# Kernel optimization log

Measured on AMD Instinct MI355X. Metric: run time of the kernel, lower is better.

The kernel has to match this reference:

```python
import jax, jax.numpy as jnp
import numpy as np

NUM_HEADS = 16
HEAD_DIM = 64


def setup_inputs() -> dict:
    key = jax.random.key(0)
    k1, k2, k3 = jax.random.split(key, 3)
    B, N, D = 4, 2048, NUM_HEADS * HEAD_DIM
    q = jax.random.normal(k1, (B, N, D), dtype=jnp.float32)
    k = jax.random.normal(k2, (B, N, D), dtype=jnp.float32)
    v = jax.random.normal(k3, (B, N, D), dtype=jnp.float32)
    # causal mask: True where attention is allowed
    attn_mask = jnp.tril(jnp.ones((N, N), dtype=bool))
    return {"q": q, "k": k, "v": v, "attn_mask": attn_mask}


def reference(q, k, v, attn_mask):
    B, N, D = q.shape
    H, Hd = NUM_HEADS, HEAD_DIM
    # [B, N, H*Hd] -> [B, H, N, Hd]
    qh = q.reshape(B, N, H, Hd).transpose(0, 2, 1, 3)
    kh = k.reshape(B, N, H, Hd).transpose(0, 2, 1, 3)
    vh = v.reshape(B, N, H, Hd).transpose(0, 2, 1, 3)
    scale = 1.0 / jnp.sqrt(jnp.asarray(Hd, dtype=q.dtype))
    scores = jnp.einsum('bhqd,bhkd->bhqk', qh, kh) * scale  # [B,H,N,N]
    scores = jnp.where(attn_mask[None, None, :, :], scores, -jnp.inf)
    probs = jax.nn.softmax(scores, axis=-1)
    y = jnp.einsum('bhqk,bhkd->bhqd', probs, vh)  # [B,H,N,Hd]
    return y.transpose(0, 2, 1, 3).reshape(B, N, H * Hd)
```

## Files before the change

### kernel.cpp

```cpp
#include <hip/hip_runtime.h>

#define RS 1024
#define SEQLEN 2048

typedef __fp16 f16;
typedef __attribute__((ext_vector_type(2))) __fp16 half2v;
typedef __attribute__((ext_vector_type(4))) __fp16 half4v;
typedef __attribute__((ext_vector_type(8))) __fp16 half8v;
typedef __attribute__((ext_vector_type(4))) float float4v;

__device__ __forceinline__ half8v pack8h(float4v a, float4v b) {
  union { half8v v; half2v h[4]; } u;
  u.h[0] = __builtin_amdgcn_cvt_pkrtz(a[0], a[1]);
  u.h[1] = __builtin_amdgcn_cvt_pkrtz(a[2], a[3]);
  u.h[2] = __builtin_amdgcn_cvt_pkrtz(b[0], b[1]);
  u.h[3] = __builtin_amdgcn_cvt_pkrtz(b[2], b[3]);
  return u.v;
}

template<int NG, bool DOMASK>
__device__ __forceinline__ void compute_tile(
    const f16* __restrict__ Klds, const f16* __restrict__ VB,
    const half8v (&aqh)[2][2], float4v (&o)[2][4], float (&lp)[2],
    int quad, int lm, int wlm)
{
  float4v sfr[NG][4];
  #pragma unroll
  for (int i = 0; i < NG; ++i)
    #pragma unroll
    for (int nb = 0; nb < 4; ++nb)
      sfr[i][nb] = (float4v){0.f, 0.f, 0.f, 0.f};

  #pragma unroll
  for (int nb = 0; nb < 4; ++nb) {
    const int row = nb*16 + lm;
    #pragma unroll
    for (int s = 0; s < 2; ++s) {
      const half8v ak = *(const half8v*)&Klds[row*64 + (((s*4 + quad) ^ (lm & 7)) * 8)];
      #pragma unroll
      for (int i = 0; i < NG; ++i) {
        const int g = (NG == 2) ? i : 1;
        sfr[i][nb] = __builtin_amdgcn_mfma_f32_16x16x32_f16(ak, aqh[g][s], sfr[i][nb], 0, 0, 0);
      }
    }
  }

  half4v pa[NG][4];
  #pragma unroll
  for (int i = 0; i < NG; ++i) {
    const int g = (NG == 2) ? i : 1;
    const bool m = DOMASK && (NG == 1 || i == 0);
    float acc = 0.f;
    #pragma unroll
    for (int nb = 0; nb < 4; ++nb) {
      float p[4];
      #pragma unroll
      for (int r = 0; r < 4; ++r) {
        const int n = nb*16 + quad*4 + r;
        const float e = __builtin_amdgcn_exp2f(sfr[i][nb][r]);
        p[r] = (m && (n > wlm)) ? 0.f : e;
      }
      acc += (p[0] + p[1]) + (p[2] + p[3]);
      union { half4v v; half2v h[2]; } u;
      u.h[0] = __builtin_amdgcn_cvt_pkrtz(p[0], p[1]);
      u.h[1] = __builtin_amdgcn_cvt_pkrtz(p[2], p[3]);
      pa[i][nb] = u.v;
    }
    lp[g] += acc;
  }

  #pragma unroll
  for (int nb = 0; nb < 4; ++nb) {
    const int kvq = nb*4 + quad;
    #pragma unroll
    for (int db = 0; db < 4; ++db) {
      const half4v vb = *(const half4v*)&VB[kvq*256 + (((db*16 + lm) ^ quad) * 4)];
      #pragma unroll
      for (int i = 0; i < NG; ++i) {
        const int g = (NG == 2) ? i : 1;
        o[g][db] = __builtin_amdgcn_mfma_f32_16x16x16f16(pa[i][nb], vb, o[g][db], 0, 0, 0);
      }
    }
  }
}

__global__ __launch_bounds__(256, 2) void fa_fwd(
    const float* __restrict__ Qg, const float* __restrict__ Kg,
    const float* __restrict__ Vg, float* __restrict__ Og)
{
  __shared__ __align__(16) f16 Klds[64*64];
  __shared__ __align__(16) f16 VB[64*64];

  const int tid  = threadIdx.x;
  const int w    = tid >> 6;
  const int lane = tid & 63;
  const int quad = lane >> 4;
  const int lm   = lane & 15;
  const int wlm  = w*16 + lm;

  const int bid = blockIdx.x;
  const int bh  = bid & 63;
  const int qt  = bid >> 6;
  const int tb  = 31 - qt;

  const size_t headoff = (size_t)(bh >> 4) * SEQLEN * RS + (size_t)(bh & 15) * 64;
  const float* Kb = Kg + headoff;
  const float* Vb = Vg + headoff;

  const int rb[2] = { qt*64 + w*16, tb*64 + w*16 };

  const float qs = 0.18033688011112042f;
  half8v aqh[2][2];
  #pragma unroll
  for (int g = 0; g < 2; ++g) {
    const float* qp = Qg + headoff + (size_t)(rb[g] + lm) * RS + quad*8;
    aqh[g][0] = pack8h(*(const float4v*)qp * qs,        *(const float4v*)(qp + 4) * qs);
    aqh[g][1] = pack8h(*(const float4v*)(qp + 32) * qs, *(const float4v*)(qp + 36) * qs);
  }

  float4v o[2][4] = {};
  float lp[2] = {0.f, 0.f};

  const int krow = tid >> 3, kcb = tid & 7;
  const int rgrp = tid >> 4, dgrp = tid & 15;
  const int r3 = rgrp & 3;

  float4v pk[4], pv[4];
  auto loadKV = [&](int kv0) {
    const float* kp = Kb + (size_t)(kv0 + krow) * RS + kcb*8;
    pk[0] = *(const float4v*)kp;       pk[1] = *(const float4v*)(kp + 4);
    const float* kp2 = kp + (size_t)32 * RS;
    pk[2] = *(const float4v*)kp2;      pk[3] = *(const float4v*)(kp2 + 4);
    const float* vp = Vb + (size_t)(kv0 + rgrp*4) * RS + dgrp*4;
    pv[0] = *(const float4v*)vp;
    pv[1] = *(const float4v*)(vp + RS);
    pv[2] = *(const float4v*)(vp + 2*RS);
    pv[3] = *(const float4v*)(vp + 3*RS);
  };
  auto stageKV = [&]() {
    *(half8v*)&Klds[krow*64 + ((kcb ^ (krow & 7)) * 8)] = pack8h(pk[0], pk[1]);
    const int row2 = krow + 32;
    *(half8v*)&Klds[row2*64 + ((kcb ^ (row2 & 7)) * 8)] = pack8h(pk[2], pk[3]);
    union { half8v v8[2]; half2v h[8]; } u;
    #pragma unroll
    for (int cp = 0; cp < 4; ++cp) {
      const int c = cp ^ r3;
      u.h[cp*2]     = __builtin_amdgcn_cvt_pkrtz(pv[0][c], pv[1][c]);
      u.h[cp*2 + 1] = __builtin_amdgcn_cvt_pkrtz(pv[2][c], pv[3][c]);
    }
    f16* dst = &VB[rgrp*256 + dgrp*16];
    *(half8v*)dst       = u.v8[0];
    *(half8v*)(dst + 8) = u.v8[1];
  };

  loadKV(0); stageKV();
  const int jmax = tb;
  for (int j = 0; j <= jmax; ++j) {
    __syncthreads();
    const bool pre = (j < jmax);
    if (pre) loadKV((j + 1) * 64);
    if (j < qt)
      compute_tile<2, false>(Klds, VB, aqh, o, lp, quad, lm, wlm);
    else if (j == qt)
      compute_tile<2, true >(Klds, VB, aqh, o, lp, quad, lm, wlm);
    else if (j < jmax)
      compute_tile<1, false>(Klds, VB, aqh, o, lp, quad, lm, wlm);
    else
      compute_tile<1, true >(Klds, VB, aqh, o, lp, quad, lm, wlm);
    __syncthreads();
    if (pre) stageKV();
  }

  #pragma unroll
  for (int g = 0; g < 2; ++g) {
    float l = lp[g];
    l += __shfl_xor(l, 16);
    l += __shfl_xor(l, 32);
    const float linv = 1.0f / l;
    #pragma unroll
    for (int r = 0; r < 4; ++r) {
      const float nrm = __shfl(linv, quad*4 + r);
      float* op = Og + headoff + (size_t)(rb[g] + quad*4 + r) * RS;
      #pragma unroll
      for (int db = 0; db < 4; ++db)
        op[db*16 + lm] = o[g][db][r] * nrm;
    }
  }
}

extern "C" void kernel_launch(void* const* d_in, const int* in_sizes, int n_in,
                              void* d_out, int out_size, void* d_ws, size_t ws_size,
                              hipStream_t stream) {
  const float* q = (const float*)d_in[0];
  const float* k = (const float*)d_in[1];
  const float* v = (const float*)d_in[2];
  float* out = (float*)d_out;
  fa_fwd<<<dim3(16 * 64), dim3(256), 0, stream>>>(q, k, v, out);
}
```

Baseline: 198.7 us.

## Split paired causal query tiles into one tile per block with higher occupancy

Each block now processes a single 64-row query tile instead of a balanced pair of tiles, doubling the grid and dispatching the longest tiles first. Register usage drops, so launch bounds are raised to allow four blocks per CU. The intent is better latency hiding through occupancy and simpler control flow, at the cost of staging K/V tiles separately per query tile and so roughly doubling global K/V load and convert work.

```diff
diff --git a/kernel.cpp b/kernel.cpp
--- a/kernel.cpp
+++ b/kernel.cpp
@@ -18,18 +18,15 @@
   return u.v;
 }
 
-template<int NG, bool DOMASK>
+template<bool DOMASK>
 __device__ __forceinline__ void compute_tile(
     const f16* __restrict__ Klds, const f16* __restrict__ VB,
-    const half8v (&aqh)[2][2], float4v (&o)[2][4], float (&lp)[2],
+    const half8v (&aq)[2], float4v (&o)[4], float& lp,
     int quad, int lm, int wlm)
 {
-  float4v sfr[NG][4];
+  float4v sfr[4];
   #pragma unroll
-  for (int i = 0; i < NG; ++i)
-    #pragma unroll
-    for (int nb = 0; nb < 4; ++nb)
-      sfr[i][nb] = (float4v){0.f, 0.f, 0.f, 0.f};
+  for (int nb = 0; nb < 4; ++nb) sfr[nb] = (float4v){0.f, 0.f, 0.f, 0.f};
 
   #pragma unroll
   for (int nb = 0; nb < 4; ++nb) {
@@ -37,37 +34,28 @@
     #pragma unroll
     for (int s = 0; s < 2; ++s) {
       const half8v ak = *(const half8v*)&Klds[row*64 + (((s*4 + quad) ^ (lm & 7)) * 8)];
-      #pragma unroll
-      for (int i = 0; i < NG; ++i) {
-        const int g = (NG == 2) ? i : 1;
-        sfr[i][nb] = __builtin_amdgcn_mfma_f32_16x16x32_f16(ak, aqh[g][s], sfr[i][nb], 0, 0, 0);
-      }
+      sfr[nb] = __builtin_amdgcn_mfma_f32_16x16x32_f16(ak, aq[s], sfr[nb], 0, 0, 0);
     }
   }
 
-  half4v pa[NG][4];
+  half4v pa[4];
+  float acc = 0.f;
   #pragma unroll
-  for (int i = 0; i < NG; ++i) {
-    const int g = (NG == 2) ? i : 1;
-    const bool m = DOMASK && (NG == 1 || i == 0);
-    float acc = 0.f;
+  for (int nb = 0; nb < 4; ++nb) {
+    float p[4];
     #pragma unroll
-    for (int nb = 0; nb < 4; ++nb) {
-      float p[4];
-      #pragma unroll
-      for (int r = 0; r < 4; ++r) {
-        const int n = nb*16 + quad*4 + r;
-        const float e = __builtin_amdgcn_exp2f(sfr[i][nb][r]);
-        p[r] = (m && (n > wlm)) ? 0.f : e;
-      }
-      acc += (p[0] + p[1]) + (p[2] + p[3]);
-      union { half4v v; half2v h[2]; } u;
-      u.h[0] = __builtin_amdgcn_cvt_pkrtz(p[0], p[1]);
-      u.h[1] = __builtin_amdgcn_cvt_pkrtz(p[2], p[3]);
-      pa[i][nb] = u.v;
+    for (int r = 0; r < 4; ++r) {
+      const int n = nb*16 + quad*4 + r;
+      const float e = __builtin_amdgcn_exp2f(sfr[nb][r]);
+      p[r] = (DOMASK && (n > wlm)) ? 0.f : e;
     }
-    lp[g] += acc;
+    acc += (p[0] + p[1]) + (p[2] + p[3]);
+    union { half4v v; half2v h[2]; } u;
+    u.h[0] = __builtin_amdgcn_cvt_pkrtz(p[0], p[1]);
+    u.h[1] = __builtin_amdgcn_cvt_pkrtz(p[2], p[3]);
+    pa[nb] = u.v;
   }
+  lp += acc;
 
   #pragma unroll
   for (int nb = 0; nb < 4; ++nb) {
@@ -75,16 +63,12 @@
     #pragma unroll
     for (int db = 0; db < 4; ++db) {
       const half4v vb = *(const half4v*)&VB[kvq*256 + (((db*16 + lm) ^ quad) * 4)];
-      #pragma unroll
-      for (int i = 0; i < NG; ++i) {
-        const int g = (NG == 2) ? i : 1;
-        o[g][db] = __builtin_amdgcn_mfma_f32_16x16x16f16(pa[i][nb], vb, o[g][db], 0, 0, 0);
-      }
+      o[db] = __builtin_amdgcn_mfma_f32_16x16x16f16(pa[nb], vb, o[db], 0, 0, 0);
     }
   }
 }
 
-__global__ __launch_bounds__(256, 2) void fa_fwd(
+__global__ __launch_bounds__(256, 4) void fa_fwd(
     const float* __restrict__ Qg, const float* __restrict__ Kg,
     const float* __restrict__ Vg, float* __restrict__ Og)
 {
@@ -100,26 +84,22 @@
 
   const int bid = blockIdx.x;
   const int bh  = bid & 63;
-  const int qt  = bid >> 6;
-  const int tb  = 31 - qt;
+  const int t   = 31 - (bid >> 6);
 
   const size_t headoff = (size_t)(bh >> 4) * SEQLEN * RS + (size_t)(bh & 15) * 64;
   const float* Kb = Kg + headoff;
   const float* Vb = Vg + headoff;
 
-  const int rb[2] = { qt*64 + w*16, tb*64 + w*16 };
-
   const float qs = 0.18033688011112042f;
-  half8v aqh[2][2];
-  #pragma unroll
-  for (int g = 0; g < 2; ++g) {
-    const float* qp = Qg + headoff + (size_t)(rb[g] + lm) * RS + quad*8;
-    aqh[g][0] = pack8h(*(const float4v*)qp * qs,        *(const float4v*)(qp + 4) * qs);
-    aqh[g][1] = pack8h(*(const float4v*)(qp + 32) * qs, *(const float4v*)(qp + 36) * qs);
+  half8v aq[2];
+  {
+    const float* qp = Qg + headoff + (size_t)(t*64 + w*16 + lm) * RS + quad*8;
+    aq[0] = pack8h(*(const float4v*)qp * qs,        *(const float4v*)(qp + 4) * qs);
+    aq[1] = pack8h(*(const float4v*)(qp + 32) * qs, *(const float4v*)(qp + 36) * qs);
   }
 
-  float4v o[2][4] = {};
-  float lp[2] = {0.f, 0.f};
+  float4v o[4] = {};
+  float lp = 0.f;
 
   const int krow = tid >> 3, kcb = tid & 7;
   const int rgrp = tid >> 4, dgrp = tid & 15;
@@ -154,37 +134,28 @@
   };
 
   loadKV(0); stageKV();
-  const int jmax = tb;
-  for (int j = 0; j <= jmax; ++j) {
+  for (int j = 0; j <= t; ++j) {
     __syncthreads();
-    const bool pre = (j < jmax);
-    if (pre) loadKV((j + 1) * 64);
-    if (j < qt)
-      compute_tile<2, false>(Klds, VB, aqh, o, lp, quad, lm, wlm);
-    else if (j == qt)
-      compute_tile<2, true >(Klds, VB, aqh, o, lp, quad, lm, wlm);
-    else if (j < jmax)
-      compute_tile<1, false>(Klds, VB, aqh, o, lp, quad, lm, wlm);
+    if (j < t) loadKV((j + 1) * 64);
+    if (j < t)
+      compute_tile<false>(Klds, VB, aq, o, lp, quad, lm, wlm);
     else
-      compute_tile<1, true >(Klds, VB, aqh, o, lp, quad, lm, wlm);
+      compute_tile<true >(Klds, VB, aq, o, lp, quad, lm, wlm);
     __syncthreads();
-    if (pre) stageKV();
+    if (j < t) stageKV();
   }
 
+  float l = lp;
+  l += __shfl_xor(l, 16);
+  l += __shfl_xor(l, 32);
+  const float linv = 1.0f / l;
   #pragma unroll
-  for (int g = 0; g < 2; ++g) {
-    float l = lp[g];
-    l += __shfl_xor(l, 16);
-    l += __shfl_xor(l, 32);
-    const float linv = 1.0f / l;
+  for (int r = 0; r < 4; ++r) {
+    const float nrm = __shfl(linv, quad*4 + r);
+    float* op = Og + headoff + (size_t)(t*64 + w*16 + quad*4 + r) * RS;
     #pragma unroll
-    for (int r = 0; r < 4; ++r) {
-      const float nrm = __shfl(linv, quad*4 + r);
-      float* op = Og + headoff + (size_t)(rb[g] + quad*4 + r) * RS;
-      #pragma unroll
-      for (int db = 0; db < 4; ++db)
-        op[db*16 + lm] = o[g][db][r] * nrm;
-    }
+    for (int db = 0; db < 4; ++db)
+      op[db*16 + lm] = o[db][r] * nrm;
   }
 }
 
@@ -195,5 +166,5 @@
   const float* k = (const float*)d_in[1];
   const float* v = (const float*)d_in[2];
   float* out = (float*)d_out;
-  fa_fwd<<<dim3(16 * 64), dim3(256), 0, stream>>>(q, k, v, out);
+  fa_fwd<<<dim3(32 * 64), dim3(256), 0, stream>>>(q, k, v, out);
 }
```

Measured after the change: 195.7 us. No clear change (-1.5%).
